# Optimization experiments

Hardware: AMD Instinct MI355X
Metric: run time of the kernel (lower is better)

The kernel has to match this reference:

```python
import jax, jax.numpy as jnp
import numpy as np

B, C, H, W = 4, 192, 128, 128
NH = 6
HD = C // NH            # 32
GS = 8                  # window (group) size
K = 16                  # unfold kernel size
STRIDE, PAD = 8, 4
NUM = H // GS           # 16 groups per side
BG = B * NUM * NUM      # 1024 windows
N = GS * GS             # 64 tokens per group
KK = K * K              # 256 sampled tokens per window
SCALE = HD ** -0.5


def _rope(x):
    # lucidrains-style rotary embedding along dim -2 (positions), last dim = head_dim
    d = x.shape[-1]
    inv = 1.0 / (10000.0 ** (jnp.arange(0, d, 2, dtype=jnp.float32) / d))
    t = jnp.arange(x.shape[-2], dtype=jnp.float32)
    freqs = jnp.repeat(t[:, None] * inv[None, :], 2, axis=-1)  # [seq, d], interleaved
    cos, sin = jnp.cos(freqs), jnp.sin(freqs)
    xp = x.reshape(x.shape[:-1] + (d // 2, 2))
    xr = jnp.stack((-xp[..., 1], xp[..., 0]), axis=-1).reshape(x.shape)
    return x * cos + xr * sin


def _l2norm(x):
    # torch F.normalize(dim=-1): x / max(||x||, eps)
    n = jnp.linalg.norm(x, axis=-1, keepdims=True)
    return x / jnp.maximum(n, 1e-12)


def setup_inputs() -> dict:
    key = jax.random.key(0)
    ks = jax.random.split(key, 6)
    return {
        "x_complete": jax.random.normal(ks[0], (B, C, H, W), jnp.float32),
        "graph": jax.random.randint(ks[1], (BG, 1, N, KK), 0, 2) > 0,
        "w_group": jax.random.normal(ks[2], (C, C), jnp.float32) * 0.02,
        "b_group": jnp.zeros((C,), jnp.float32),
        "w_sample": jax.random.normal(ks[3], (2 * C, C), jnp.float32) * 0.02,
        "b_sample": jnp.zeros((2 * C,), jnp.float32),
        "w_proj": jax.random.normal(ks[4], (C, C), jnp.float32) * 0.02,
        "b_proj": jnp.zeros((C,), jnp.float32),
    }


def reference(x_complete, graph, w_group, b_group, w_sample, b_sample, w_proj, b_proj):
    # --- local grouping: [B,C,(numh sh),(numw sw)] -> [(B numh numw), sh*sw, C]
    xg = x_complete.reshape(B, C, NUM, GS, NUM, GS).transpose(0, 2, 4, 3, 5, 1).reshape(BG, N, C)
    # --- proj_group: 1x1 Conv1d over channels, then split heads 'b (h c) n -> b h n c'
    x1 = jnp.einsum('bnc,dc->bnd', xg, w_group) + b_group
    x1 = x1.reshape(BG, N, NH, HD).transpose(0, 2, 1, 3)            # [BG,NH,N,HD]
    # --- proj_sample: 1x1 Conv2d to 2C channels
    xs = jnp.einsum('bchw,dc->bdhw', x_complete, w_sample) + b_sample[None, :, None, None]
    # --- F.unfold(kernel=16, stride=8, pad=4): patch features channel-major (c,k0,k1)
    patches = jax.lax.conv_general_dilated_patches(
        xs, (K, K), (STRIDE, STRIDE), ((PAD, PAD), (PAD, PAD)))    # [B, 2C*KK, NUM, NUM]
    xs = patches.reshape(B, 2 * C, KK, NUM * NUM).transpose(0, 3, 2, 1).reshape(BG, KK, 2 * C)
    # --- 'b n (div h c) -> div b h n c'
    xs = xs.reshape(BG, KK, 2, NH, HD)
    x2 = xs[:, :, 0].transpose(0, 2, 1, 3)                          # [BG,NH,KK,HD]
    feat = xs[:, :, 1].transpose(0, 2, 1, 3)                        # [BG,NH,KK,HD]
    # --- RoPE + masked cosine-sim attention
    q = _rope(x1)
    k = _rope(x2)
    sim = jnp.einsum('bhmc,bhnc->bhmn', _l2norm(q), _l2norm(k))
    sim = sim + (-100.0) * (~graph).astype(sim.dtype)
    corr = jax.nn.softmax(sim * SCALE, axis=-1)                     # [BG,NH,N,KK]
    out = jnp.einsum('bhmn,bhnc->bhmc', corr, feat)                 # [BG,NH,N,HD]
    out = out.transpose(0, 2, 1, 3).reshape(BG, N, C)
    return out @ w_proj.T + b_proj
```

## Files before the change

kernel.cpp:

```cpp
#include <hip/hip_runtime.h>
#include <hip/hip_bf16.h>

#define B_    4
#define C_    192
#define C2_   384
#define PIX_  16384
#define NH_   6
#define BG_   1024
#define SCALE_ 0.17677669529663687f
#define C1_ 0.2550348943f

typedef __attribute__((ext_vector_type(8))) short short8v;
typedef __attribute__((ext_vector_type(4))) float f32x4;

__global__ __launch_bounds__(256, 1)
void k_rope_init(float2* __restrict__ tbl) {
    int e = blockIdx.x * 256 + threadIdx.x;
    if (e >= 4096) return;
    int pos = e >> 4, j = e & 15;
    float freq = powf(10.0f, -0.25f * (float)j);
    float ang = (float)pos * freq;
    float sn, cs;
    sincosf(ang, &sn, &cs);
    tbl[e] = make_float2(cs, sn);
}

__global__ __launch_bounds__(256, 4)
void k_gmask(const int* __restrict__ g, unsigned int* __restrict__ gbits) {
    int e = blockIdx.x * 256 + threadIdx.x;
    const uint4* p = (const uint4*)(g + (size_t)e * 32);
    unsigned int m = 0u;
#pragma unroll
    for (int i = 0; i < 8; ++i) {
        uint4 v = p[i];
        m |= (v.x ? 1u : 0u) << (i * 4);
        m |= (v.y ? 1u : 0u) << (i * 4 + 1);
        m |= (v.z ? 1u : 0u) << (i * 4 + 2);
        m |= (v.w ? 1u : 0u) << (i * 4 + 3);
    }
    gbits[e] = m;
}

__global__ __launch_bounds__(256, 4)
void k_wcast(const float* __restrict__ wsm, const float* __restrict__ wgb,
             const float* __restrict__ wpj, __hip_bfloat16* __restrict__ wb)
{
    int e = (blockIdx.x * 256 + threadIdx.x) * 4;
    float4 v = (e < 73728) ? *(const float4*)(wsm + e)
             : (e < 110592) ? *(const float4*)(wgb + (e - 73728))
                            : *(const float4*)(wpj + (e - 110592));
    union { uint2 u; __hip_bfloat16 h[4]; } pk;
    pk.h[0] = __float2bfloat16(v.x); pk.h[1] = __float2bfloat16(v.y);
    pk.h[2] = __float2bfloat16(v.z); pk.h[3] = __float2bfloat16(v.w);
    *(uint2*)(wb + e) = pk.u;
}

__global__ __launch_bounds__(256, 4)
void k_convm(const float* __restrict__ x, const __hip_bfloat16* __restrict__ wb,
             const float* __restrict__ bsm, const float* __restrict__ bgb,
             const float2* __restrict__ tbl,
             __hip_bfloat16* __restrict__ xsk, __hip_bfloat16* __restrict__ xsv,
             __hip_bfloat16* __restrict__ qbf)
{
    __shared__ __align__(16) char smem[25600];
    const int bid0 = blockIdx.x;
    const int bid = (bid0 & 7) * 384 + (bid0 >> 3);
    const int ogrp = bid % 3;
    const int pb   = bid / 3;
    const int b = pb >> 8, pt = pb & 255;
    const int px0 = pt * 64;
    const int t = threadIdx.x;

    {
        const int px = t & 63, cq = t >> 6;
        const float* src = x + ((size_t)b * C_ + cq * 48) * PIX_ + px0 + px;
        char* row = smem + px * 400 + cq * 96;
#pragma unroll
        for (int i = 0; i < 6; ++i) {
            union { uint4 u; __hip_bfloat16 h[8]; } pk;
#pragma unroll
            for (int j = 0; j < 8; ++j)
                pk.h[j] = __float2bfloat16(src[(size_t)(i * 8 + j) * PIX_]);
            *(uint4*)(row + i * 16) = pk.u;
        }
    }
    __syncthreads();

    const int w = t >> 6, lane = t & 63;
    const int l15 = lane & 15, g = lane >> 4;
    const int mb = (w & 1) * 32;
    const int nb = (w >> 1) * 32;

    short8v a0r[6], a1r[6];
#pragma unroll
    for (int ks = 0; ks < 6; ++ks) {
        a0r[ks] = *(const short8v*)(smem + (mb + l15) * 400      + ks * 64 + g * 16);
        a1r[ks] = *(const short8v*)(smem + (mb + 16 + l15) * 400 + ks * 64 + g * 16);
    }

    float* ot = (float*)smem;
    const f32x4 zz = {0.0f, 0.0f, 0.0f, 0.0f};

    if (ogrp == 1) {
#pragma unroll
        for (int o2 = 0; o2 < 3; ++o2) {
            const int oct = 3 + o2;
            f32x4 acc00 = zz, acc01 = zz, acc10 = zz, acc11 = zz;
            const __hip_bfloat16* w0 = wb + (size_t)(oct * 64 + nb + l15) * C_;
            const __hip_bfloat16* w1 = w0 + 16 * C_;
#pragma unroll
            for (int ks = 0; ks < 6; ++ks) {
                const short8v b0 = *(const short8v*)(w0 + ks * 32 + g * 8);
                const short8v b1 = *(const short8v*)(w1 + ks * 32 + g * 8);
                acc00 = __builtin_amdgcn_mfma_f32_16x16x32_bf16(a0r[ks], b0, acc00, 0, 0, 0);
                acc01 = __builtin_amdgcn_mfma_f32_16x16x32_bf16(a0r[ks], b1, acc01, 0, 0, 0);
                acc10 = __builtin_amdgcn_mfma_f32_16x16x32_bf16(a1r[ks], b0, acc10, 0, 0, 0);
                acc11 = __builtin_amdgcn_mfma_f32_16x16x32_bf16(a1r[ks], b1, acc11, 0, 0, 0);
            }
            const float bo0 = bsm[oct * 64 + nb + l15];
            const float bo1 = bsm[oct * 64 + nb + 16 + l15];
            union { uint2 u; __hip_bfloat16 h[4]; } p00, p10, p01, p11;
#pragma unroll
            for (int j = 0; j < 4; ++j) {
                p00.h[j] = __float2bfloat16(acc00[j] + bo0);
                p10.h[j] = __float2bfloat16(acc10[j] + bo0);
                p01.h[j] = __float2bfloat16(acc01[j] + bo1);
                p11.h[j] = __float2bfloat16(acc11[j] + bo1);
            }
            __hip_bfloat16* d0 = xsv + (size_t)(b * C_ + o2 * 64 + nb + l15) * PIX_
                                     + px0 + mb + g * 4;
            *(uint2*)d0        = p00.u;
            *(uint2*)(d0 + 16) = p10.u;
            __hip_bfloat16* d1 = d0 + (size_t)16 * PIX_;
            *(uint2*)d1        = p01.u;
            *(uint2*)(d1 + 16) = p11.u;
        }
        return;
    }

    __syncthreads();

    for (int o2 = 0; o2 < 3; ++o2) {
        const int oct = (ogrp == 0) ? o2 : 6 + o2;
        f32x4 acc00 = zz, acc01 = zz, acc10 = zz, acc11 = zz;
        const __hip_bfloat16* w0 = wb + (size_t)(oct * 64 + nb + l15) * C_;
        const __hip_bfloat16* w1 = w0 + 16 * C_;
#pragma unroll
        for (int ks = 0; ks < 6; ++ks) {
            const short8v b0 = *(const short8v*)(w0 + ks * 32 + g * 8);
            const short8v b1 = *(const short8v*)(w1 + ks * 32 + g * 8);
            acc00 = __builtin_amdgcn_mfma_f32_16x16x32_bf16(a0r[ks], b0, acc00, 0, 0, 0);
            acc01 = __builtin_amdgcn_mfma_f32_16x16x32_bf16(a0r[ks], b1, acc01, 0, 0, 0);
            acc10 = __builtin_amdgcn_mfma_f32_16x16x32_bf16(a1r[ks], b0, acc10, 0, 0, 0);
            acc11 = __builtin_amdgcn_mfma_f32_16x16x32_bf16(a1r[ks], b1, acc11, 0, 0, 0);
        }
        __syncthreads();

#pragma unroll
        for (int j = 0; j < 4; ++j) {
            ot[(mb + g * 4 + j) * 68      + nb + l15]      = acc00[j];
            ot[(mb + 16 + g * 4 + j) * 68 + nb + l15]      = acc10[j];
            ot[(mb + g * 4 + j) * 68      + nb + 16 + l15] = acc01[j];
            ot[(mb + 16 + g * 4 + j) * 68 + nb + 16 + l15] = acc11[j];
        }
        __syncthreads();

        if (ogrp == 0) {
            const int px = t >> 2, i = t & 3;
            const int ocb = oct * 64 + i * 16;
            float v[16];
#pragma unroll
            for (int q4 = 0; q4 < 4; ++q4) {
                float4 vv = *(const float4*)&ot[px * 68 + i * 16 + q4 * 4];
                float4 bv = *(const float4*)(bsm + ocb + q4 * 4);
                v[q4 * 4 + 0] = vv.x + bv.x; v[q4 * 4 + 1] = vv.y + bv.y;
                v[q4 * 4 + 2] = vv.z + bv.z; v[q4 * 4 + 3] = vv.w + bv.w;
            }
            float n2 = 0.0f;
#pragma unroll
            for (int d = 0; d < 16; ++d) n2 = fmaf(v[d], v[d], n2);
            n2 += __shfl_xor(n2, 1);
            const float inv = 1.0f / fmaxf(sqrtf(n2), 1e-12f);
            union { uint4 u[2]; __hip_bfloat16 h[16]; } pk;
#pragma unroll
            for (int d = 0; d < 16; ++d) pk.h[d] = __float2bfloat16(v[d] * inv);
            __hip_bfloat16* dst = xsk + ((size_t)b * PIX_ + px0 + px) * C_ + ocb;
            *(uint4*)dst       = pk.u[0];
            *(uint4*)(dst + 8) = pk.u[1];
        } else {
            const int px = t & 63, hh = t >> 6;
            if (hh < 2) {
                const int p = px0 + px;
                const int r = p >> 7, c = p & 127;
                const int n = (r & 7) * 8 + (c & 7);
                const int bg = (b << 8) + ((r >> 3) << 4) + (c >> 3);
                const int hglob = (oct - 6) * 2 + hh;
                float v[32];
#pragma unroll
                for (int d4 = 0; d4 < 8; ++d4) {
                    float4 vv = *(const float4*)&ot[px * 68 + hh * 32 + d4 * 4];
                    float4 bv = *(const float4*)(bgb + hglob * 32 + d4 * 4);
                    v[d4 * 4 + 0] = vv.x + bv.x; v[d4 * 4 + 1] = vv.y + bv.y;
                    v[d4 * 4 + 2] = vv.z + bv.z; v[d4 * 4 + 3] = vv.w + bv.w;
                }
                float rr[32];
#pragma unroll
                for (int j = 0; j < 16; ++j) {
                    float2 cs = tbl[n * 16 + j];
                    float a0 = v[2 * j], a1 = v[2 * j + 1];
                    rr[2 * j]     = a0 * cs.x - a1 * cs.y;
                    rr[2 * j + 1] = a1 * cs.x + a0 * cs.y;
                }
                float n2 = 0.0f;
#pragma unroll
                for (int d = 0; d < 32; ++d) n2 = fmaf(rr[d], rr[d], n2);
                const float inv = 1.0f / fmaxf(sqrtf(n2), 1e-12f);
                __hip_bfloat16* dst = qbf + ((size_t)(bg * NH_ + hglob) * 64 + n) * 32;
#pragma unroll
                for (int c8 = 0; c8 < 4; ++c8) {
                    union { uint4 u; __hip_bfloat16 h[8]; } pk;
#pragma unroll
                    for (int i = 0; i < 8; ++i) pk.h[i] = __float2bfloat16(rr[c8 * 8 + i] * inv);
                    *(uint4*)(dst + c8 * 8) = pk.u;
                }
            }
        }
    }
}

__global__ __launch_bounds__(512, 2)
void k_attn(const __hip_bfloat16* __restrict__ xsk, const __hip_bfloat16* __restrict__ xsv,
            const unsigned int* __restrict__ gbits, const __hip_bfloat16* __restrict__ qb,
            const float2* __restrict__ tbl, float* __restrict__ attn)
{
    __shared__ __align__(16) char smem[52736];
    const int bid0 = blockIdx.x;
    const int bid = (bid0 & 7) * 768 + (bid0 >> 3);
    const int h = bid % NH_;
    const int bg = bid / NH_;
    const int b = bg >> 8, ph = (bg >> 4) & 15, pw = bg & 15;
    const int t = threadIdx.x;
    const int w = t >> 6, lane = t & 63;
    const int g = lane >> 4, l15 = lane & 15;
    const int rbase = (w & 3) * 16;
    const int wcol  = w >> 2;
    const int cb    = wcol * 128;
    const int cb32  = wcol * 4;

    const short8v qa = *(const short8v*)(qb +
        ((size_t)(bg * NH_ + h) * 64 + rbase + l15) * 32 + g * 8);

    {
        const int m = t >> 1, half = t & 1;
        const int k0 = m >> 4, k1 = m & 15;
        const int rr = ph * 8 - 4 + k0, cc = pw * 8 - 4 + k1;
        const bool inb = ((unsigned)rr < 128u) && ((unsigned)cc < 128u);
        float kv[16];
        if (inb) {
            const uint4* pk = (const uint4*)(xsk +
                ((size_t)b * PIX_ + rr * 128 + cc) * C_ + h * 32 + half * 16);
            union { uint4 u; __hip_bfloat16 h8[8]; } r0, r1;
            r0.u = pk[0]; r1.u = pk[1];
#pragma unroll
            for (int d = 0; d < 8; ++d) {
                kv[d]     = __bfloat162float(r0.h8[d]);
                kv[8 + d] = __bfloat162float(r1.h8[d]);
            }
        } else {
#pragma unroll
            for (int d = 0; d < 16; ++d) kv[d] = 0.0f;
        }
        union { uint4 u; __hip_bfloat16 hh[8]; } p0, p1;
#pragma unroll
        for (int p = 0; p < 8; ++p) {
            float2 cs = tbl[m * 16 + half * 8 + p];
            float a0 = kv[2 * p], a1 = kv[2 * p + 1];
            float e0 = a0 * cs.x - a1 * cs.y;
            float e1 = a1 * cs.x + a0 * cs.y;
            if (p < 4) { p0.hh[2 * p] = __float2bfloat16(e0); p0.hh[2 * p + 1] = __float2bfloat16(e1); }
            else { p1.hh[2 * (p - 4)] = __float2bfloat16(e0); p1.hh[2 * (p - 4) + 1] = __float2bfloat16(e1); }
        }
        *(uint4*)(smem + m * 80 + half * 32)      = p0.u;
        *(uint4*)(smem + m * 80 + half * 32 + 16) = p1.u;
    }

    {
        const int d = t & 31, k0 = t >> 5;
        const int rr = ph * 8 - 4 + k0;
        const int c0 = pw * 8 - 4;
        char* dst = smem + 34816 + d * 528 + k0 * 32;
        const __hip_bfloat16* src = xsv + (size_t)(b * C_ + h * 32 + d) * PIX_ + rr * 128 + c0;
        const bool rok = (unsigned)rr < 128u;
        if (rok && pw >= 1 && pw <= 14) {
            const uint2* s2 = (const uint2*)src;
            uint2 a0 = s2[0], a1 = s2[1], a2 = s2[2], a3 = s2[3];
            ((uint4*)dst)[0] = make_uint4(a0.x, a0.y, a1.x, a1.y);
            ((uint4*)dst)[1] = make_uint4(a2.x, a2.y, a3.x, a3.y);
        } else {
            __hip_bfloat16* dh = (__hip_bfloat16*)dst;
            __hip_bfloat16 z = __float2bfloat16(0.0f);
#pragma unroll
            for (int i = 0; i < 16; ++i) {
                bool ok = rok && ((unsigned)(c0 + i) < 128u);
                dh[i] = ok ? src[i] : z;
            }
        }
    }

    {
        unsigned int* gbl = (unsigned int*)(smem + 20480);
        const int q = t >> 3, wd = t & 7;
        gbl[q * 9 + wd] = gbits[(size_t)bg * 512 + t];
    }
    __syncthreads();

    f32x4 acc[8];
    const f32x4 zz = {0.0f, 0.0f, 0.0f, 0.0f};
#pragma unroll
    for (int tile = 0; tile < 8; ++tile) {
        const short8v kb = *(const short8v*)(smem + (cb + tile * 16 + l15) * 80 + g * 16);
        acc[tile] = __builtin_amdgcn_mfma_f32_16x16x32_bf16(qa, kb, zz, 0, 0, 0);
    }

    const unsigned int* gbl = (const unsigned int*)(smem + 20480);
    float* reds = (float*)(smem + 51712);
    float sm4[4], inv4[4];
#pragma unroll
    for (int j = 0; j < 4; ++j) {
        const int q = rbase + g * 4 + j;
        const unsigned int wv[4] = { gbl[q * 9 + cb32], gbl[q * 9 + cb32 + 1],
                                     gbl[q * 9 + cb32 + 2], gbl[q * 9 + cb32 + 3] };
        float sm = 0.0f;
#pragma unroll
        for (int tile = 0; tile < 8; ++tile) {
            const unsigned int bit = (wv[tile >> 1] >> ((tile & 1) * 16 + l15)) & 1u;
            float e = __builtin_amdgcn_exp2f(fmaf(acc[tile][j], C1_, -C1_));
            e = bit ? e : 0.0f;
            acc[tile][j] = e;
            sm += e;
        }
        sm += __shfl_xor(sm, 1);
        sm += __shfl_xor(sm, 2);
        sm += __shfl_xor(sm, 4);
        sm += __shfl_xor(sm, 8);
        sm4[j] = sm;
        if (l15 == 0) reds[wcol * 64 + q] = sm;
    }
    __syncthreads();
#pragma unroll
    for (int j = 0; j < 4; ++j) {
        const int q = rbase + g * 4 + j;
        inv4[j] = 1.0f / (sm4[j] + reds[(wcol ^ 1) * 64 + q] + 1e-37f);
    }

    char* plw = smem + w * 4352;
#pragma unroll
    for (int tile = 0; tile < 8; ++tile)
#pragma unroll
        for (int j = 0; j < 4; ++j) {
            *(__hip_bfloat16*)(plw + (g * 4 + j) * 272 + (tile * 16 + l15) * 2) =
                __float2bfloat16(acc[tile][j]);
        }

    f32x4 o0 = zz, o1 = zz;
#pragma unroll
    for (int ks = 0; ks < 4; ++ks) {
        const short8v pa  = *(const short8v*)(plw + l15 * 272 + (ks * 32 + g * 8) * 2);
        const short8v vb0 = *(const short8v*)(smem + 34816 + l15 * 528        + (cb + ks * 32 + g * 8) * 2);
        const short8v vb1 = *(const short8v*)(smem + 34816 + (16 + l15) * 528 + (cb + ks * 32 + g * 8) * 2);
        o0 = __builtin_amdgcn_mfma_f32_16x16x32_bf16(pa, vb0, o0, 0, 0, 0);
        o1 = __builtin_amdgcn_mfma_f32_16x16x32_bf16(pa, vb1, o1, 0, 0, 0);
    }
    __syncthreads();

    float* ob = (float*)smem;
    if (wcol == 1) {
#pragma unroll
        for (int j = 0; j < 4; ++j) {
            const int q = rbase + g * 4 + j;
            ob[q * 33 + l15]      = o0[j];
            ob[q * 33 + 16 + l15] = o1[j];
        }
    }
    __syncthreads();
    if (wcol == 0) {
#pragma unroll
        for (int j = 0; j < 4; ++j) {
            const int q = rbase + g * 4 + j;
            float v0 = (o0[j] + ob[q * 33 + l15])      * inv4[j];
            float v1 = (o1[j] + ob[q * 33 + 16 + l15]) * inv4[j];
            attn[((size_t)bg * 64 + q) * 192 + h * 32 + l15]      = v0;
            attn[((size_t)bg * 64 + q) * 192 + h * 32 + 16 + l15] = v1;
        }
    }
}

__global__ __launch_bounds__(256, 4)
void k_oprojm(const float* __restrict__ attn, const __hip_bfloat16* __restrict__ wpb,
              const float* __restrict__ bp, float* __restrict__ out)
{
    __shared__ __align__(16) char smem[25600];
    const int bid0 = blockIdx.x;
    const int bid = (bid0 & 7) * 384 + (bid0 >> 3);
    const int oct = bid % 3;
    const int rt  = bid / 3;
    const int row0 = rt * 64;
    const int t = threadIdx.x;

#pragma unroll
    for (int e0 = 0; e0 < 12; ++e0) {
        const int e = e0 * 256 + t;
        const int r = e / 48, c4 = e % 48;
        float4 v = *(const float4*)(attn + (size_t)(row0 + r) * 192 + c4 * 4);
        union { uint2 u; __hip_bfloat16 h[4]; } pk;
        pk.h[0] = __float2bfloat16(v.x); pk.h[1] = __float2bfloat16(v.y);
        pk.h[2] = __float2bfloat16(v.z); pk.h[3] = __float2bfloat16(v.w);
        *(uint2*)(smem + r * 400 + c4 * 8) = pk.u;
    }
    __syncthreads();

    const int w = t >> 6, lane = t & 63;
    const int l15 = lane & 15, g = lane >> 4;
    const int mb = (w & 1) * 32;
    const int nb = (w >> 1) * 32;

    const f32x4 zz = {0.0f, 0.0f, 0.0f, 0.0f};
    f32x4 acc00 = zz, acc01 = zz, acc10 = zz, acc11 = zz;
    const __hip_bfloat16* w0 = wpb + (size_t)(oct * 64 + nb + l15) * C_;
    const __hip_bfloat16* w1 = w0 + 16 * C_;
#pragma unroll
    for (int ks = 0; ks < 6; ++ks) {
        const short8v a0 = *(const short8v*)(smem + (mb + l15) * 400      + ks * 64 + g * 16);
        const short8v a1 = *(const short8v*)(smem + (mb + 16 + l15) * 400 + ks * 64 + g * 16);
        const short8v b0 = *(const short8v*)(w0 + ks * 32 + g * 8);
        const short8v b1 = *(const short8v*)(w1 + ks * 32 + g * 8);
        acc00 = __builtin_amdgcn_mfma_f32_16x16x32_bf16(a0, b0, acc00, 0, 0, 0);
        acc01 = __builtin_amdgcn_mfma_f32_16x16x32_bf16(a0, b1, acc01, 0, 0, 0);
        acc10 = __builtin_amdgcn_mfma_f32_16x16x32_bf16(a1, b0, acc10, 0, 0, 0);
        acc11 = __builtin_amdgcn_mfma_f32_16x16x32_bf16(a1, b1, acc11, 0, 0, 0);
    }
    __syncthreads();

    float* ot = (float*)smem;
#pragma unroll
    for (int j = 0; j < 4; ++j) {
        ot[(mb + g * 4 + j) * 68      + nb + l15]      = acc00[j];
        ot[(mb + 16 + g * 4 + j) * 68 + nb + l15]      = acc10[j];
        ot[(mb + g * 4 + j) * 68      + nb + 16 + l15] = acc01[j];
        ot[(mb + 16 + g * 4 + j) * 68 + nb + 16 + l15] = acc11[j];
    }
    __syncthreads();

    {
        const int k = t & 15, pxi = t >> 4;
        const float4 bias4 = *(const float4*)(bp + oct * 64 + k * 4);
#pragma unroll
        for (int p = 0; p < 4; ++p) {
            const int px = p * 16 + pxi;
            float4 v = *(const float4*)&ot[px * 68 + k * 4];
            v.x += bias4.x; v.y += bias4.y; v.z += bias4.z; v.w += bias4.w;
            *(float4*)(out + (size_t)(row0 + px) * 192 + oct * 64 + k * 4) = v;
        }
    }
}

extern "C" void kernel_launch(void* const* d_in, const int* in_sizes, int n_in,
                              void* d_out, int out_size, void* d_ws, size_t ws_size,
                              hipStream_t stream)
{
    (void)in_sizes; (void)n_in; (void)out_size; (void)ws_size;
    const float* x   = (const float*)d_in[0];
    const int* grph  = (const int*)d_in[1];
    const float* wg  = (const float*)d_in[2];
    const float* bgb = (const float*)d_in[3];
    const float* wsm = (const float*)d_in[4];
    const float* bsm = (const float*)d_in[5];
    const float* wp  = (const float*)d_in[6];
    const float* bp  = (const float*)d_in[7];
    float* out = (float*)d_out;

    char* wsb = (char*)d_ws;
    __hip_bfloat16* xsk = (__hip_bfloat16*)wsb;
    __hip_bfloat16* xsv = (__hip_bfloat16*)(wsb + 25165824ull);
    __hip_bfloat16* qbf = (__hip_bfloat16*)(wsb + 50331648ull);
    float2* tbl = (float2*)(wsb + 75497472ull);
    unsigned int* gbits = (unsigned int*)(wsb + 75530240ull);
    __hip_bfloat16* wb  = (__hip_bfloat16*)(wsb + 77627392ull);
    __hip_bfloat16* wpb = wb + 110592;

    hipLaunchKernelGGL(k_rope_init, dim3(16),   dim3(256), 0, stream, tbl);
    hipLaunchKernelGGL(k_wcast,     dim3(144),  dim3(256), 0, stream, wsm, wg, wp, wb);
    hipLaunchKernelGGL(k_gmask,     dim3(2048), dim3(256), 0, stream, grph, gbits);
    hipLaunchKernelGGL(k_convm,     dim3(3072), dim3(256), 0, stream, x, wb, bsm, bgb, tbl, xsk, xsv, qbf);
    hipLaunchKernelGGL(k_attn,      dim3(6144), dim3(512), 0, stream, xsk, xsv, gbits, qbf, tbl, out);
    hipLaunchKernelGGL(k_oprojm,    dim3(3072), dim3(256), 0, stream, out, wpb, bp, out);
}
```

Before: 205.0 us.

## Merge convm output groups into one block and normalize directly from MFMA registers

Each k_convm block now computes all three output groups (V, normalized K, RoPE+normalized Q) for its 64-pixel tile, so the x tile is loaded and bf16-converted once instead of three times. For K and Q the MFMA operands are swapped so each lane holds channel-contiguous results, letting bias, RoPE and the L2 norm be done in registers with cross-lane shuffles instead of staging through shared memory with extra barriers. The grid shrinks from 3072 to 1024 blocks, which lowers parallelism and lengthens per-block work, and the output stores become narrower 8-byte writes.

```diff
diff --git a/kernel.cpp b/kernel.cpp
--- a/kernel.cpp
+++ b/kernel.cpp
@@ -63,11 +63,8 @@
              __hip_bfloat16* __restrict__ qbf)
 {
     __shared__ __align__(16) char smem[25600];
-    const int bid0 = blockIdx.x;
-    const int bid = (bid0 & 7) * 384 + (bid0 >> 3);
-    const int ogrp = bid % 3;
-    const int pb   = bid / 3;
-    const int b = pb >> 8, pt = pb & 255;
+    const int bid = blockIdx.x;
+    const int b = bid >> 8, pt = bid & 255;
     const int px0 = pt * 64;
     const int t = threadIdx.x;
 
@@ -91,57 +88,18 @@
     const int mb = (w & 1) * 32;
     const int nb = (w >> 1) * 32;
 
-    short8v a0r[6], a1r[6];
+    short8v xf0[6], xf1[6];
 #pragma unroll
     for (int ks = 0; ks < 6; ++ks) {
-        a0r[ks] = *(const short8v*)(smem + (mb + l15) * 400      + ks * 64 + g * 16);
-        a1r[ks] = *(const short8v*)(smem + (mb + 16 + l15) * 400 + ks * 64 + g * 16);
-    }
-
-    float* ot = (float*)smem;
+        xf0[ks] = *(const short8v*)(smem + (mb + l15) * 400      + ks * 64 + g * 16);
+        xf1[ks] = *(const short8v*)(smem + (mb + 16 + l15) * 400 + ks * 64 + g * 16);
+    }
+
     const f32x4 zz = {0.0f, 0.0f, 0.0f, 0.0f};
 
-    if (ogrp == 1) {
-#pragma unroll
-        for (int o2 = 0; o2 < 3; ++o2) {
-            const int oct = 3 + o2;
-            f32x4 acc00 = zz, acc01 = zz, acc10 = zz, acc11 = zz;
-            const __hip_bfloat16* w0 = wb + (size_t)(oct * 64 + nb + l15) * C_;
-            const __hip_bfloat16* w1 = w0 + 16 * C_;
-#pragma unroll
-            for (int ks = 0; ks < 6; ++ks) {
-                const short8v b0 = *(const short8v*)(w0 + ks * 32 + g * 8);
-                const short8v b1 = *(const short8v*)(w1 + ks * 32 + g * 8);
-                acc00 = __builtin_amdgcn_mfma_f32_16x16x32_bf16(a0r[ks], b0, acc00, 0, 0, 0);
-                acc01 = __builtin_amdgcn_mfma_f32_16x16x32_bf16(a0r[ks], b1, acc01, 0, 0, 0);
-                acc10 = __builtin_amdgcn_mfma_f32_16x16x32_bf16(a1r[ks], b0, acc10, 0, 0, 0);
-                acc11 = __builtin_amdgcn_mfma_f32_16x16x32_bf16(a1r[ks], b1, acc11, 0, 0, 0);
-            }
-            const float bo0 = bsm[oct * 64 + nb + l15];
-            const float bo1 = bsm[oct * 64 + nb + 16 + l15];
-            union { uint2 u; __hip_bfloat16 h[4]; } p00, p10, p01, p11;
-#pragma unroll
-            for (int j = 0; j < 4; ++j) {
-                p00.h[j] = __float2bfloat16(acc00[j] + bo0);
-                p10.h[j] = __float2bfloat16(acc10[j] + bo0);
-                p01.h[j] = __float2bfloat16(acc01[j] + bo1);
-                p11.h[j] = __float2bfloat16(acc11[j] + bo1);
-            }
-            __hip_bfloat16* d0 = xsv + (size_t)(b * C_ + o2 * 64 + nb + l15) * PIX_
-                                     + px0 + mb + g * 4;
-            *(uint2*)d0        = p00.u;
-            *(uint2*)(d0 + 16) = p10.u;
-            __hip_bfloat16* d1 = d0 + (size_t)16 * PIX_;
-            *(uint2*)d1        = p01.u;
-            *(uint2*)(d1 + 16) = p11.u;
-        }
-        return;
-    }
-
-    __syncthreads();
-
+#pragma unroll
     for (int o2 = 0; o2 < 3; ++o2) {
-        const int oct = (ogrp == 0) ? o2 : 6 + o2;
+        const int oct = 3 + o2;
         f32x4 acc00 = zz, acc01 = zz, acc10 = zz, acc11 = zz;
         const __hip_bfloat16* w0 = wb + (size_t)(oct * 64 + nb + l15) * C_;
         const __hip_bfloat16* w1 = w0 + 16 * C_;
@@ -149,82 +107,153 @@
         for (int ks = 0; ks < 6; ++ks) {
             const short8v b0 = *(const short8v*)(w0 + ks * 32 + g * 8);
             const short8v b1 = *(const short8v*)(w1 + ks * 32 + g * 8);
-            acc00 = __builtin_amdgcn_mfma_f32_16x16x32_bf16(a0r[ks], b0, acc00, 0, 0, 0);
-            acc01 = __builtin_amdgcn_mfma_f32_16x16x32_bf16(a0r[ks], b1, acc01, 0, 0, 0);
-            acc10 = __builtin_amdgcn_mfma_f32_16x16x32_bf16(a1r[ks], b0, acc10, 0, 0, 0);
-            acc11 = __builtin_amdgcn_mfma_f32_16x16x32_bf16(a1r[ks], b1, acc11, 0, 0, 0);
-        }
-        __syncthreads();
-
-#pragma unroll
-        for (int j = 0; j < 4; ++j) {
-            ot[(mb + g * 4 + j) * 68      + nb + l15]      = acc00[j];
-            ot[(mb + 16 + g * 4 + j) * 68 + nb + l15]      = acc10[j];
-            ot[(mb + g * 4 + j) * 68      + nb + 16 + l15] = acc01[j];
-            ot[(mb + 16 + g * 4 + j) * 68 + nb + 16 + l15] = acc11[j];
-        }
-        __syncthreads();
-
-        if (ogrp == 0) {
-            const int px = t >> 2, i = t & 3;
-            const int ocb = oct * 64 + i * 16;
-            float v[16];
-#pragma unroll
-            for (int q4 = 0; q4 < 4; ++q4) {
-                float4 vv = *(const float4*)&ot[px * 68 + i * 16 + q4 * 4];
-                float4 bv = *(const float4*)(bsm + ocb + q4 * 4);
-                v[q4 * 4 + 0] = vv.x + bv.x; v[q4 * 4 + 1] = vv.y + bv.y;
-                v[q4 * 4 + 2] = vv.z + bv.z; v[q4 * 4 + 3] = vv.w + bv.w;
-            }
-            float n2 = 0.0f;
-#pragma unroll
-            for (int d = 0; d < 16; ++d) n2 = fmaf(v[d], v[d], n2);
-            n2 += __shfl_xor(n2, 1);
-            const float inv = 1.0f / fmaxf(sqrtf(n2), 1e-12f);
-            union { uint4 u[2]; __hip_bfloat16 h[16]; } pk;
-#pragma unroll
-            for (int d = 0; d < 16; ++d) pk.h[d] = __float2bfloat16(v[d] * inv);
-            __hip_bfloat16* dst = xsk + ((size_t)b * PIX_ + px0 + px) * C_ + ocb;
-            *(uint4*)dst       = pk.u[0];
-            *(uint4*)(dst + 8) = pk.u[1];
-        } else {
-            const int px = t & 63, hh = t >> 6;
-            if (hh < 2) {
-                const int p = px0 + px;
-                const int r = p >> 7, c = p & 127;
-                const int n = (r & 7) * 8 + (c & 7);
-                const int bg = (b << 8) + ((r >> 3) << 4) + (c >> 3);
-                const int hglob = (oct - 6) * 2 + hh;
-                float v[32];
-#pragma unroll
-                for (int d4 = 0; d4 < 8; ++d4) {
-                    float4 vv = *(const float4*)&ot[px * 68 + hh * 32 + d4 * 4];
-                    float4 bv = *(const float4*)(bgb + hglob * 32 + d4 * 4);
-                    v[d4 * 4 + 0] = vv.x + bv.x; v[d4 * 4 + 1] = vv.y + bv.y;
-                    v[d4 * 4 + 2] = vv.z + bv.z; v[d4 * 4 + 3] = vv.w + bv.w;
-                }
-                float rr[32];
-#pragma unroll
-                for (int j = 0; j < 16; ++j) {
-                    float2 cs = tbl[n * 16 + j];
-                    float a0 = v[2 * j], a1 = v[2 * j + 1];
-                    rr[2 * j]     = a0 * cs.x - a1 * cs.y;
-                    rr[2 * j + 1] = a1 * cs.x + a0 * cs.y;
-                }
-                float n2 = 0.0f;
-#pragma unroll
-                for (int d = 0; d < 32; ++d) n2 = fmaf(rr[d], rr[d], n2);
-                const float inv = 1.0f / fmaxf(sqrtf(n2), 1e-12f);
-                __hip_bfloat16* dst = qbf + ((size_t)(bg * NH_ + hglob) * 64 + n) * 32;
-#pragma unroll
-                for (int c8 = 0; c8 < 4; ++c8) {
-                    union { uint4 u; __hip_bfloat16 h[8]; } pk;
-#pragma unroll
-                    for (int i = 0; i < 8; ++i) pk.h[i] = __float2bfloat16(rr[c8 * 8 + i] * inv);
-                    *(uint4*)(dst + c8 * 8) = pk.u;
-                }
-            }
-        }
+            acc00 = __builtin_amdgcn_mfma_f32_16x16x32_bf16(xf0[ks], b0, acc00, 0, 0, 0);
+            acc01 = __builtin_amdgcn_mfma_f32_16x16x32_bf16(xf0[ks], b1, acc01, 0, 0, 0);
+            acc10 = __builtin_amdgcn_mfma_f32_16x16x32_bf16(xf1[ks], b0, acc10, 0, 0, 0);
+            acc11 = __builtin_amdgcn_mfma_f32_16x16x32_bf16(xf1[ks], b1, acc11, 0, 0, 0);
+        }
+        const float bo0 = bsm[oct * 64 + nb + l15];
+        const float bo1 = bsm[oct * 64 + nb + 16 + l15];
+        union { uint2 u; __hip_bfloat16 h[4]; } p00, p10, p01, p11;
+#pragma unroll
+        for (int j = 0; j < 4; ++j) {
+            p00.h[j] = __float2bfloat16(acc00[j] + bo0);
+            p10.h[j] = __float2bfloat16(acc10[j] + bo0);
+            p01.h[j] = __float2bfloat16(acc01[j] + bo1);
+            p11.h[j] = __float2bfloat16(acc11[j] + bo1);
+        }
+        __hip_bfloat16* d0 = xsv + (size_t)(b * C_ + o2 * 64 + nb + l15) * PIX_
+                                 + px0 + mb + g * 4;
+        *(uint2*)d0        = p00.u;
+        *(uint2*)(d0 + 16) = p10.u;
+        __hip_bfloat16* d1 = d0 + (size_t)16 * PIX_;
+        *(uint2*)d1        = p01.u;
+        *(uint2*)(d1 + 16) = p11.u;
+    }
+
+#pragma unroll
+    for (int o2 = 0; o2 < 3; ++o2) {
+        const int oct = o2;
+        f32x4 a00 = zz, a01 = zz, a10 = zz, a11 = zz;
+        const __hip_bfloat16* w0 = wb + (size_t)(oct * 64 + nb + l15) * C_;
+        const __hip_bfloat16* w1 = w0 + 16 * C_;
+#pragma unroll
+        for (int ks = 0; ks < 6; ++ks) {
+            const short8v wf0 = *(const short8v*)(w0 + ks * 32 + g * 8);
+            const short8v wf1 = *(const short8v*)(w1 + ks * 32 + g * 8);
+            a00 = __builtin_amdgcn_mfma_f32_16x16x32_bf16(wf0, xf0[ks], a00, 0, 0, 0);
+            a01 = __builtin_amdgcn_mfma_f32_16x16x32_bf16(wf0, xf1[ks], a01, 0, 0, 0);
+            a10 = __builtin_amdgcn_mfma_f32_16x16x32_bf16(wf1, xf0[ks], a10, 0, 0, 0);
+            a11 = __builtin_amdgcn_mfma_f32_16x16x32_bf16(wf1, xf1[ks], a11, 0, 0, 0);
+        }
+        const float4 bv0 = *(const float4*)(bsm + oct * 64 + nb + g * 4);
+        const float4 bv1 = *(const float4*)(bsm + oct * 64 + nb + 16 + g * 4);
+        a00[0] += bv0.x; a00[1] += bv0.y; a00[2] += bv0.z; a00[3] += bv0.w;
+        a01[0] += bv0.x; a01[1] += bv0.y; a01[2] += bv0.z; a01[3] += bv0.w;
+        a10[0] += bv1.x; a10[1] += bv1.y; a10[2] += bv1.z; a10[3] += bv1.w;
+        a11[0] += bv1.x; a11[1] += bv1.y; a11[2] += bv1.z; a11[3] += bv1.w;
+        float s0 = 0.0f, s1 = 0.0f;
+#pragma unroll
+        for (int j = 0; j < 4; ++j) {
+            s0 = fmaf(a00[j], a00[j], s0); s0 = fmaf(a10[j], a10[j], s0);
+            s1 = fmaf(a01[j], a01[j], s1); s1 = fmaf(a11[j], a11[j], s1);
+        }
+        s0 += __shfl_xor(s0, 16); s0 += __shfl_xor(s0, 32);
+        s1 += __shfl_xor(s1, 16); s1 += __shfl_xor(s1, 32);
+        const float inv0 = 1.0f / fmaxf(sqrtf(s0), 1e-12f);
+        const float inv1 = 1.0f / fmaxf(sqrtf(s1), 1e-12f);
+        union { uint2 u; __hip_bfloat16 h[4]; } q00, q10, q01, q11;
+#pragma unroll
+        for (int j = 0; j < 4; ++j) {
+            q00.h[j] = __float2bfloat16(a00[j] * inv0);
+            q10.h[j] = __float2bfloat16(a10[j] * inv0);
+            q01.h[j] = __float2bfloat16(a01[j] * inv1);
+            q11.h[j] = __float2bfloat16(a11[j] * inv1);
+        }
+        __hip_bfloat16* d0 = xsk + ((size_t)b * PIX_ + px0 + mb + l15) * C_
+                                 + oct * 64 + nb + g * 4;
+        *(uint2*)d0        = q00.u;
+        *(uint2*)(d0 + 16) = q10.u;
+        __hip_bfloat16* d1 = d0 + (size_t)16 * C_;
+        *(uint2*)d1        = q01.u;
+        *(uint2*)(d1 + 16) = q11.u;
+    }
+
+    const int r = pt >> 1;
+    const int c0q = (pt & 1) * 64 + mb + l15;
+    const int n0 = (r & 7) * 8 + (c0q & 7);
+    const int n1 = (r & 7) * 8 + ((c0q + 16) & 7);
+    const int bg0 = (b << 8) + ((r >> 3) << 4) + (c0q >> 3);
+    const int bg1 = (b << 8) + ((r >> 3) << 4) + ((c0q + 16) >> 3);
+#pragma unroll
+    for (int o2 = 0; o2 < 3; ++o2) {
+        const int oct = 6 + o2;
+        f32x4 a00 = zz, a01 = zz, a10 = zz, a11 = zz;
+        const __hip_bfloat16* w0 = wb + (size_t)(oct * 64 + nb + l15) * C_;
+        const __hip_bfloat16* w1 = w0 + 16 * C_;
+#pragma unroll
+        for (int ks = 0; ks < 6; ++ks) {
+            const short8v wf0 = *(const short8v*)(w0 + ks * 32 + g * 8);
+            const short8v wf1 = *(const short8v*)(w1 + ks * 32 + g * 8);
+            a00 = __builtin_amdgcn_mfma_f32_16x16x32_bf16(wf0, xf0[ks], a00, 0, 0, 0);
+            a01 = __builtin_amdgcn_mfma_f32_16x16x32_bf16(wf0, xf1[ks], a01, 0, 0, 0);
+            a10 = __builtin_amdgcn_mfma_f32_16x16x32_bf16(wf1, xf0[ks], a10, 0, 0, 0);
+            a11 = __builtin_amdgcn_mfma_f32_16x16x32_bf16(wf1, xf1[ks], a11, 0, 0, 0);
+        }
+        const float4 bv0 = *(const float4*)(bgb + (oct - 6) * 64 + nb + g * 4);
+        const float4 bv1 = *(const float4*)(bgb + (oct - 6) * 64 + nb + 16 + g * 4);
+        a00[0] += bv0.x; a00[1] += bv0.y; a00[2] += bv0.z; a00[3] += bv0.w;
+        a01[0] += bv0.x; a01[1] += bv0.y; a01[2] += bv0.z; a01[3] += bv0.w;
+        a10[0] += bv1.x; a10[1] += bv1.y; a10[2] += bv1.z; a10[3] += bv1.w;
+        a11[0] += bv1.x; a11[1] += bv1.y; a11[2] += bv1.z; a11[3] += bv1.w;
+        {
+            float2 cA, cB;
+            cA = tbl[n0 * 16 + g * 2]; cB = tbl[n0 * 16 + g * 2 + 1];
+            { float u0 = a00[0], u1 = a00[1];
+              a00[0] = u0 * cA.x - u1 * cA.y; a00[1] = u1 * cA.x + u0 * cA.y; }
+            { float u0 = a00[2], u1 = a00[3];
+              a00[2] = u0 * cB.x - u1 * cB.y; a00[3] = u1 * cB.x + u0 * cB.y; }
+            cA = tbl[n0 * 16 + 8 + g * 2]; cB = tbl[n0 * 16 + 8 + g * 2 + 1];
+            { float u0 = a10[0], u1 = a10[1];
+              a10[0] = u0 * cA.x - u1 * cA.y; a10[1] = u1 * cA.x + u0 * cA.y; }
+            { float u0 = a10[2], u1 = a10[3];
+              a10[2] = u0 * cB.x - u1 * cB.y; a10[3] = u1 * cB.x + u0 * cB.y; }
+            cA = tbl[n1 * 16 + g * 2]; cB = tbl[n1 * 16 + g * 2 + 1];
+            { float u0 = a01[0], u1 = a01[1];
+              a01[0] = u0 * cA.x - u1 * cA.y; a01[1] = u1 * cA.x + u0 * cA.y; }
+            { float u0 = a01[2], u1 = a01[3];
+              a01[2] = u0 * cB.x - u1 * cB.y; a01[3] = u1 * cB.x + u0 * cB.y; }
+            cA = tbl[n1 * 16 + 8 + g * 2]; cB = tbl[n1 * 16 + 8 + g * 2 + 1];
+            { float u0 = a11[0], u1 = a11[1];
+              a11[0] = u0 * cA.x - u1 * cA.y; a11[1] = u1 * cA.x + u0 * cA.y; }
+            { float u0 = a11[2], u1 = a11[3];
+              a11[2] = u0 * cB.x - u1 * cB.y; a11[3] = u1 * cB.x + u0 * cB.y; }
+        }
+        float s0 = 0.0f, s1 = 0.0f;
+#pragma unroll
+        for (int j = 0; j < 4; ++j) {
+            s0 = fmaf(a00[j], a00[j], s0); s0 = fmaf(a10[j], a10[j], s0);
+            s1 = fmaf(a01[j], a01[j], s1); s1 = fmaf(a11[j], a11[j], s1);
+        }
+        s0 += __shfl_xor(s0, 16); s0 += __shfl_xor(s0, 32);
+        s1 += __shfl_xor(s1, 16); s1 += __shfl_xor(s1, 32);
+        const float inv0 = 1.0f / fmaxf(sqrtf(s0), 1e-12f);
+        const float inv1 = 1.0f / fmaxf(sqrtf(s1), 1e-12f);
+        union { uint2 u; __hip_bfloat16 h[4]; } q00, q10, q01, q11;
+#pragma unroll
+        for (int j = 0; j < 4; ++j) {
+            q00.h[j] = __float2bfloat16(a00[j] * inv0);
+            q10.h[j] = __float2bfloat16(a10[j] * inv0);
+            q01.h[j] = __float2bfloat16(a01[j] * inv1);
+            q11.h[j] = __float2bfloat16(a11[j] * inv1);
+        }
+        const int hglob = (oct - 6) * 2 + (nb >> 5);
+        __hip_bfloat16* d0 = qbf + (((size_t)bg0 * NH_ + hglob) * 64 + n0) * 32 + g * 4;
+        *(uint2*)d0        = q00.u;
+        *(uint2*)(d0 + 16) = q10.u;
+        __hip_bfloat16* d1 = qbf + (((size_t)bg1 * NH_ + hglob) * 64 + n1) * 32 + g * 4;
+        *(uint2*)d1        = q01.u;
+        *(uint2*)(d1 + 16) = q11.u;
     }
 }
 
@@ -491,7 +520,7 @@
     hipLaunchKernelGGL(k_rope_init, dim3(16),   dim3(256), 0, stream, tbl);
     hipLaunchKernelGGL(k_wcast,     dim3(144),  dim3(256), 0, stream, wsm, wg, wp, wb);
     hipLaunchKernelGGL(k_gmask,     dim3(2048), dim3(256), 0, stream, grph, gbits);
-    hipLaunchKernelGGL(k_convm,     dim3(3072), dim3(256), 0, stream, x, wb, bsm, bgb, tbl, xsk, xsv, qbf);
+    hipLaunchKernelGGL(k_convm,     dim3(1024), dim3(256), 0, stream, x, wb, bsm, bgb, tbl, xsk, xsv, qbf);
     hipLaunchKernelGGL(k_attn,      dim3(6144), dim3(512), 0, stream, xsk, xsv, gbits, qbf, tbl, out);
     hipLaunchKernelGGL(k_oprojm,    dim3(3072), dim3(256), 0, stream, out, wpb, bp, out);
 }
```

After: 187.4 us. -8.6%, faster.
